# Performance work log

Measured on AMD Instinct MI355X. Metric: run time of the kernel, lower is better.

## Reference

```python
import jax, jax.numpy as jnp
import numpy as np
from math import sqrt

D_MODEL = 1024
N_HEADS = 16
FFN = 4096
B, N = 2, 2048
EPS = 1e-5


def _layernorm(x, g, b):
    mu = jnp.mean(x, -1, keepdims=True)
    var = jnp.mean((x - mu) ** 2, -1, keepdims=True)
    return (x - mu) * jax.lax.rsqrt(var + EPS) * g + b


def setup_inputs() -> dict:
    key = jax.random.key(0)
    ks = jax.random.split(key, 12)
    s = 1.0 / sqrt(D_MODEL)
    sf = 1.0 / sqrt(FFN)
    inp = {
        "tgt": jax.random.normal(ks[0], (B, N, D_MODEL), jnp.float32),
        # True = masked. Causal: query i may attend to keys j <= i.
        "tgt_mask": jnp.triu(jnp.ones((N, N), jnp.bool_), k=1),
        "tgt_key_pad_mask": jnp.zeros((B, N), jnp.bool_),
        "Wq": jax.random.uniform(ks[1], (D_MODEL, D_MODEL), jnp.float32, -s, s),
        "Wk": jax.random.uniform(ks[2], (D_MODEL, D_MODEL), jnp.float32, -s, s),
        "Wv": jax.random.uniform(ks[3], (D_MODEL, D_MODEL), jnp.float32, -s, s),
        "Wo": jax.random.uniform(ks[4], (D_MODEL, D_MODEL), jnp.float32, -s, s),
        "bo": jax.random.uniform(ks[5], (D_MODEL,), jnp.float32, -s, s),
        "W1": jax.random.uniform(ks[6], (FFN, D_MODEL), jnp.float32, -s, s),
        "b1": jax.random.uniform(ks[7], (FFN,), jnp.float32, -s, s),
        "W2": jax.random.uniform(ks[8], (D_MODEL, FFN), jnp.float32, -sf, sf),
        "b2": jax.random.uniform(ks[9], (D_MODEL,), jnp.float32, -sf, sf),
        "g1": jnp.ones((D_MODEL,), jnp.float32),
        "beta1": jnp.zeros((D_MODEL,), jnp.float32),
        "g2": jnp.ones((D_MODEL,), jnp.float32),
        "beta2": jnp.zeros((D_MODEL,), jnp.float32),
    }
    return inp


def _mha(x, tgt_mask, pad_mask, Wq, Wk, Wv, Wo, bo):
    b, n, d = x.shape
    dk = d // N_HEADS
    q = (x @ Wq.T).reshape(b, n, N_HEADS, dk).transpose(0, 2, 1, 3)  # bhnd
    k = (x @ Wk.T).reshape(b, n, N_HEADS, dk).transpose(0, 2, 1, 3)
    v = (x @ Wv.T).reshape(b, n, N_HEADS, dk).transpose(0, 2, 1, 3)
    scores = jnp.einsum("bhqd,bhkd->bhqk", q, k) / sqrt(dk)
    mask = tgt_mask[None, None, :, :] | pad_mask[:, None, None, :]
    scores = jnp.where(mask, -jnp.inf, scores)
    att = jax.nn.softmax(scores, axis=-1)
    out = jnp.einsum("bhqk,bhkd->bhqd", att, v).transpose(0, 2, 1, 3).reshape(b, n, d)
    return out @ Wo.T + bo


def reference(tgt, tgt_mask, tgt_key_pad_mask, Wq, Wk, Wv, Wo, bo,
              W1, b1, W2, b2, g1, beta1, g2, beta2):
    # PostNorm logic (pre_norm=False), dropout=0 (eval)
    h = _mha(tgt, tgt_mask, tgt_key_pad_mask, Wq, Wk, Wv, Wo, bo)
    x = _layernorm(tgt + h, g1, beta1)
    m = jax.nn.gelu(x @ W1.T + b1, approximate=True) @ W2.T + b2
    return _layernorm(x + m, g2, beta2)
```

## Files before the change

kernel.cpp:

```cpp
#include <hip/hip_runtime.h>


#define DEV __device__ __forceinline__

typedef __attribute__((ext_vector_type(4)))  float f32x4;
typedef __attribute__((ext_vector_type(16))) float f32x16;
typedef __attribute__((ext_vector_type(8)))  short s16x8;

static constexpr int Bb   = 2;
static constexpr int NN   = 2048;
static constexpr int DM   = 1024;
static constexpr int HH   = 16;
static constexpr int DK   = 64;
static constexpr int FF   = 4096;
static constexpr int ROWS = Bb * NN;

#define AS1(p) ((const __attribute__((address_space(1))) void*)(p))
#define AS3(p) ((__attribute__((address_space(3))) void*)(p))

DEV unsigned short f2bf(float f) {
  unsigned u = __float_as_uint(f);
  u += 0x7fff + ((u >> 16) & 1);
  return (unsigned short)(u >> 16);
}
DEV float fexp2(float x) {
  float r;
  asm("v_exp_f32 %0, %1" : "=v"(r) : "v"(x));
  return r;
}
DEV unsigned cvtpk(float lo, float hi) {
  unsigned r;
  asm("v_cvt_pk_bf16_f32 %0, %1, %2" : "=v"(r) : "v"(lo), "v"(hi));
  return r;
}

__global__ __launch_bounds__(256) void k_cast7(
    const float* __restrict__ tgt, const float* __restrict__ Wq,
    const float* __restrict__ Wk, const float* __restrict__ Wv,
    const float* __restrict__ Wo, const float* __restrict__ W1,
    const float* __restrict__ W2,
    ushort* __restrict__ xb, ushort* __restrict__ wqb,
    ushort* __restrict__ w1b, ushort* __restrict__ w2b) {
  const int i = blockIdx.x * 256 + threadIdx.x;
  constexpr int S0 = 1048576;
  constexpr int S1 = 262144;
  const float4* src;
  ushort* dstp;
  if (i < S0)               { src = (const float4*)tgt + i;            dstp = xb  + (size_t)i * 4; }
  else if (i < S0 + S1)     { src = (const float4*)Wq + (i - S0);      dstp = wqb + (size_t)(i - S0) * 4; }
  else if (i < S0 + 2 * S1) { src = (const float4*)Wk + (i - S0 - S1); dstp = wqb + (size_t)(i - S0) * 4; }
  else if (i < S0 + 3 * S1) { src = (const float4*)Wv + (i - S0 - 2 * S1); dstp = wqb + (size_t)(i - S0) * 4; }
  else if (i < S0 + 4 * S1) { src = (const float4*)Wo + (i - S0 - 3 * S1); dstp = wqb + (size_t)(i - S0) * 4; }
  else if (i < 3 * S0)      { src = (const float4*)W1 + (i - 2 * S0);  dstp = w1b + (size_t)(i - 2 * S0) * 4; }
  else                      { src = (const float4*)W2 + (i - 3 * S0);  dstp = w2b + (size_t)(i - 3 * S0) * 4; }
  float4 v = *src;
  ushort4 o;
  o.x = f2bf(v.x); o.y = f2bf(v.y); o.z = f2bf(v.z); o.w = f2bf(v.w);
  *reinterpret_cast<ushort4*>(dstp) = o;
}

template <int EPI, int BN, bool QKV, int SPLITK>
__global__ __launch_bounds__(256) void k_gemm(
    const ushort* __restrict__ A, const ushort* __restrict__ Bt,
    const float* __restrict__ bias, const float* __restrict__ resid,
    ushort* __restrict__ Cb, float* __restrict__ Cf,
    int K, int nbx) {
  __shared__ ushort As[2][128][32];
  __shared__ ushort Bs[2][BN][32];

  const int t = threadIdx.x;
  const int lane = t & 63, w = t >> 6;
  const int lr = lane & 15, lg = lane >> 4;
  const int lrow = lane >> 2, lc8 = (lane & 3) * 8;

  const int nwg = gridDim.x;
  const int bid = blockIdx.x;
  const int q8 = nwg >> 3, r8 = nwg & 7;
  const int xcd = bid & 7, lin = bid >> 3;
  int wg = (xcd < r8 ? xcd * (q8 + 1) : r8 * (q8 + 1) + (xcd - r8) * q8) + lin;
  int kc = 0;
  if constexpr (SPLITK == 2) { kc = wg & 1; wg >>= 1; }
  const int band = wg / (4 * nbx);
  const int inn  = wg % (4 * nbx);
  const int by = band * 4 + (inn & 3);
  const int bx = inn >> 2;

  const int bRow = by * 128;
  const int bCol = bx * BN;
  const int Kc = K / SPLITK;
  const int kofs = kc * Kc;
  const int nk = Kc / 32;

  constexpr int NW = BN / 32;
  const int wRow = (w >> 1) * 64, wCol = (w & 1) * (BN / 2);

  const f32x4 zero = {0.f, 0.f, 0.f, 0.f};
  f32x4 acc[4][NW];
#pragma unroll
  for (int m = 0; m < 4; ++m)
#pragma unroll
    for (int n = 0; n < NW; ++n) acc[m][n] = zero;

  auto stage = [&](int buf, int tile) {
    const int kb = kofs + tile * 32;
#pragma unroll
    for (int i = 0; i < 2; ++i) {
      int rr = w * 32 + i * 16;
      __builtin_amdgcn_global_load_lds(
          AS1(A + (size_t)(bRow + rr + lrow) * K + kb + lc8),
          AS3(&As[buf][rr][0]), 16, 0, 0);
    }
#pragma unroll
    for (int i = 0; i < BN / 64; ++i) {
      int rr = w * (BN / 4) + i * 16;
      __builtin_amdgcn_global_load_lds(
          AS1(Bt + (size_t)(bCol + rr + lrow) * K + kb + lc8),
          AS3(&Bs[buf][rr][0]), 16, 0, 0);
    }
  };

  stage(0, 0);
  for (int tt = 0; tt < nk; ++tt) {
    const int cur = tt & 1;
    if (tt + 1 < nk) {
      stage(cur ^ 1, tt + 1);
      if constexpr (BN == 128) asm volatile("s_waitcnt vmcnt(4)" ::: "memory");
      else                     asm volatile("s_waitcnt vmcnt(3)" ::: "memory");
    } else {
      asm volatile("s_waitcnt vmcnt(0)" ::: "memory");
    }
    __builtin_amdgcn_s_barrier();
    __builtin_amdgcn_sched_barrier(0);

    s16x8 af[4], bfr[NW];
#pragma unroll
    for (int m = 0; m < 4; ++m)
      af[m] = *reinterpret_cast<const s16x8*>(&As[cur][wRow + m * 16 + lr][lg * 8]);
#pragma unroll
    for (int n = 0; n < NW; ++n)
      bfr[n] = *reinterpret_cast<const s16x8*>(&Bs[cur][wCol + n * 16 + lr][lg * 8]);
#pragma unroll
    for (int m = 0; m < 4; ++m)
#pragma unroll
      for (int n = 0; n < NW; ++n)
        acc[m][n] = __builtin_amdgcn_mfma_f32_16x16x32_bf16(af[m], bfr[n], acc[m][n], 0, 0, 0);

    asm volatile("s_waitcnt lgkmcnt(0)" ::: "memory");
    __builtin_amdgcn_s_barrier();
    __builtin_amdgcn_sched_barrier(0);
  }

  ushort* CbOut = Cb;
  int colBase = bCol, Ncols = nbx * BN, third = 0;
  if (QKV) {
    third = bCol >> 10;
    CbOut = Cb + (size_t)third * ROWS * DM;
    colBase = bCol & 1023;
    Ncols = DM;
  }
#pragma unroll
  for (int m = 0; m < 4; ++m) {
    int gr = bRow + wRow + m * 16 + lg * 4;
#pragma unroll
    for (int n = 0; n < NW; ++n) {
      int gc = colBase + wCol + n * 16 + lr;
      if (QKV && third == 2) {
        int h = gc >> 6, d = gc & 63;
        int b = gr >> 11, ntok = gr & (NN - 1);
        size_t basev = ((size_t)(b * HH + h) * DK + d) * NN;
        int nb = ntok & ~63, c = (ntok >> 3) & 7, j0 = ntok & 7;
        ushort4 ov;
        ov.x = f2bf(acc[m][n][0]);
        ov.y = f2bf(acc[m][n][1]);
        ov.z = f2bf(acc[m][n][2]);
        ov.w = f2bf(acc[m][n][3]);
        ushort* VT = Cb + (size_t)3 * ROWS * DM;
        *reinterpret_cast<ushort4*>(VT + basev + nb + ((c ^ (d & 7)) << 3) + j0) = ov;
        continue;
      }
      float bv = (EPI == 1 || EPI == 2) ? bias[gc] : 0.0f;
#pragma unroll
      for (int r = 0; r < 4; ++r) {
        int nr = gr + r;
        float v = acc[m][n][r] + bv;
        if (EPI == 3) {
          Cf[((size_t)kc * ROWS + nr) * Ncols + gc] = v;
        } else if (EPI == 2) {
          size_t idx = (size_t)nr * Ncols + gc;
          Cf[idx] = v + resid[idx];
        } else if (EPI == 1) {
          size_t idx = (size_t)nr * Ncols + gc;
          float u = v + 0.044715f * v * v * v;
          float g = v / (1.0f + __expf(-1.5957691216057308f * u));
          CbOut[idx] = f2bf(g);
        } else {
          int gcs = gc;
          if (QKV && third == 1)
            gcs = (gc & ~63) | ((gc ^ ((nr & 7) << 3)) & 63);
          CbOut[(size_t)nr * Ncols + gcs] = f2bf(v);
        }
      }
    }
  }
}

template <int WB, int RED>
__global__ __launch_bounds__(256) void k_ln(const float* __restrict__ in,
                                            const float* __restrict__ p0,
                                            const float* __restrict__ p1,
                                            const float* __restrict__ pb,
                                            const float* __restrict__ g,
                                            const float* __restrict__ bta,
                                            float* __restrict__ outf,
                                            ushort* __restrict__ outb) {
  const int row = blockIdx.x;
  const int t = threadIdx.x;
  float4 v = reinterpret_cast<const float4*>(in + (size_t)row * DM)[t];
  if (RED) {
    float4 a = reinterpret_cast<const float4*>(p0 + (size_t)row * DM)[t];
    float4 b = reinterpret_cast<const float4*>(p1 + (size_t)row * DM)[t];
    float4 c = reinterpret_cast<const float4*>(pb)[t];
    v.x += a.x + b.x + c.x;
    v.y += a.y + b.y + c.y;
    v.z += a.z + b.z + c.z;
    v.w += a.w + b.w + c.w;
  }
  float s1 = v.x + v.y + v.z + v.w;
  float s2 = v.x * v.x + v.y * v.y + v.z * v.z + v.w * v.w;
#pragma unroll
  for (int m = 32; m; m >>= 1) {
    s1 += __shfl_xor(s1, m, 64);
    s2 += __shfl_xor(s2, m, 64);
  }
  __shared__ float red[2][4];
  if ((t & 63) == 0) { red[0][t >> 6] = s1; red[1][t >> 6] = s2; }
  __syncthreads();
  s1 = red[0][0] + red[0][1] + red[0][2] + red[0][3];
  s2 = red[1][0] + red[1][1] + red[1][2] + red[1][3];
  const float mu = s1 * (1.0f / DM);
  const float var = s2 * (1.0f / DM) - mu * mu;
  const float rstd = rsqrtf(var + 1e-5f);
  float4 gv = reinterpret_cast<const float4*>(g)[t];
  float4 bv = reinterpret_cast<const float4*>(bta)[t];
  float4 o;
  o.x = (v.x - mu) * rstd * gv.x + bv.x;
  o.y = (v.y - mu) * rstd * gv.y + bv.y;
  o.z = (v.z - mu) * rstd * gv.z + bv.z;
  o.w = (v.w - mu) * rstd * gv.w + bv.w;
  reinterpret_cast<float4*>(outf + (size_t)row * DM)[t] = o;
  if (WB) {
    ushort4 ob;
    ob.x = f2bf(o.x); ob.y = f2bf(o.y); ob.z = f2bf(o.z); ob.w = f2bf(o.w);
    reinterpret_cast<ushort4*>(outb + (size_t)row * DM)[t] = ob;
  }
}

static __device__ const unsigned char SCHED40[40][2] = {
  {15,0},{15,1},{15,2},{15,3}, {14,0},{14,1},{14,2},{14,3},
  {13,0},{13,1},{13,2},{13,3}, {12,0},{12,1},{12,2},{12,3},
  {11,0},{11,1},{11,2}, {10,0},{10,1},{10,2},
  {9,0},{9,1},{9,2}, {8,0},{8,1},{8,2},
  {7,0},{7,1}, {6,0},{6,1}, {5,0},{5,1}, {4,0},{4,1},
  {3,0},{2,0},{1,0},{0,0}};

__global__ __launch_bounds__(256) void k_attn(const ushort* __restrict__ Q,
                                              const ushort* __restrict__ Kb,
                                              const ushort* __restrict__ vT,
                                              ushort* __restrict__ O,
                                              float* __restrict__ Op,
                                              float* __restrict__ ml) {
  __shared__ ushort Ks[2][64 * 64];
  __shared__ ushort Vs[2][64 * 64];

  const int t = threadIdx.x;
  const int bid = blockIdx.x;
  const int xcd = bid & 7, j = bid >> 3;
  const int head = j & 3, e = j >> 2;
  const int qi = SCHED40[e][0], seg = SCHED40[e][1];
  const int bh = xcd * 4 + head;
  const int ntiles = 2 * qi + 2;
  const int nseg = (2 * qi + 9) >> 3;
  const int tb = ntiles / nseg, rem = ntiles % nseg;
  const int kt0 = seg * tb + (seg < rem ? seg : rem);
  const int kt1 = kt0 + tb + (seg < rem ? 1 : 0);

  const int lane = t & 63, wid = t >> 6;
  const int l31 = lane & 31, hi = lane >> 5;
  const int q0w = qi * 128 + wid * 32;
  const size_t qbase = ((size_t)(bh >> 4) * NN) * DM + (bh & 15) * DK;
  const size_t vbase = (size_t)bh * DK * NN;

  const float C = 0.18033688011112043f;

  s16x8 qf[4];
#pragma unroll
  for (int c = 0; c < 4; ++c)
    qf[c] = *reinterpret_cast<const s16x8*>(Q + qbase + (size_t)(q0w + l31) * DM + c * 16 + hi * 8);

  float mrun = -1e30f, lrun = 0.f, negcm = 1e30f;
  f32x16 accO[2];
#pragma unroll
  for (int dt = 0; dt < 2; ++dt)
#pragma unroll
    for (int r = 0; r < 16; ++r) accO[dt][r] = 0.f;

  auto stage = [&](int buf, int kt) {
    const int kk = kt * 64;
#pragma unroll
    for (int i = 0; i < 2; ++i) {
      int row0 = wid * 16 + i * 8;
      __builtin_amdgcn_global_load_lds(
          AS1(Kb + qbase + (size_t)(kk + row0 + (lane >> 3)) * DM + (lane & 7) * 8),
          AS3(&Ks[buf][row0 * 64]), 16, 0, 0);
      __builtin_amdgcn_global_load_lds(
          AS1(vT + vbase + (size_t)(row0 + (lane >> 3)) * NN + kk + (lane & 7) * 8),
          AS3(&Vs[buf][row0 * 64]), 16, 0, 0);
    }
  };

  stage(0, kt0);
  for (int kt = kt0, li = 0; kt < kt1; ++kt, ++li) {
    const int cur = li & 1;
    const int kk = kt * 64;
    __syncthreads();
    if (kt + 1 < kt1) stage(cur ^ 1, kt + 1);

    if (kk <= q0w + 31) {
      const char* KsB = (const char*)Ks[cur];
      const char* VsB = (const char*)Vs[cur];
      const bool diag = (kk + 64 > q0w);
      const int nsub = (kk + 32 <= q0w + 31) ? 2 : 1;

      f32x16 st[2];
      __builtin_amdgcn_s_setprio(1);
#pragma unroll
      for (int sub = 0; sub < 2; ++sub) {
        if (sub >= nsub) break;
#pragma unroll
        for (int r = 0; r < 16; ++r) st[sub][r] = 0.f;
        const int row = sub * 32 + l31;
        const int swz = (row & 7) << 4;
#pragma unroll
        for (int c = 0; c < 4; ++c) {
          s16x8 kf = *reinterpret_cast<const s16x8*>(KsB + row * 128 + ((c * 32 + hi * 16) ^ swz));
          st[sub] = __builtin_amdgcn_mfma_f32_32x32x16_bf16(kf, qf[c], st[sub], 0, 0, 0);
        }
      }
      __builtin_amdgcn_s_setprio(0);

      const int q = q0w + l31;
      float p[32];
#pragma unroll
      for (int sub = 0; sub < 2; ++sub) {
        if (sub >= nsub) break;
#pragma unroll
        for (int r = 0; r < 16; ++r) {
          float v = st[sub][r];
          if (diag) {
            int kl = sub * 32 + (r & 3) + 8 * (r >> 2) + 4 * hi;
            if (kk + kl > q) v = -1e30f;
          }
          p[sub * 16 + r] = v;
        }
      }
      float a[16];
#pragma unroll
      for (int i = 0; i < 16; ++i) a[i] = (nsub == 2) ? fmaxf(p[i], p[i + 16]) : p[i];
#pragma unroll
      for (int s = 8; s; s >>= 1)
#pragma unroll
        for (int i = 0; i < 8; ++i) if (i < s) a[i] = fmaxf(a[i], a[i + s]);
      float rm = fmaxf(a[0], __shfl_xor(a[0], 32, 64));

      if (__any(rm > mrun)) {
        const float mn = fmaxf(mrun, rm);
        const float alpha = fexp2(C * (mrun - mn));
        mrun = mn;
        negcm = -C * mn;
        lrun *= alpha;
#pragma unroll
        for (int dt = 0; dt < 2; ++dt) accO[dt] *= alpha;
      }

#pragma unroll
      for (int sub = 0; sub < 2; ++sub) {
        if (sub >= nsub) break;
#pragma unroll
        for (int i = 0; i < 16; ++i)
          p[sub * 16 + i] = fexp2(fmaf(p[sub * 16 + i], C, negcm));
      }
#pragma unroll
      for (int i = 0; i < 16; ++i) a[i] = (nsub == 2) ? (p[i] + p[i + 16]) : p[i];
#pragma unroll
      for (int s = 8; s; s >>= 1)
#pragma unroll
        for (int i = 0; i < 8; ++i) if (i < s) a[i] += a[i + s];
      lrun += a[0] + __shfl_xor(a[0], 32, 64);

      s16x8 pf[4];
#pragma unroll
      for (int sub = 0; sub < 2; ++sub) {
        if (sub >= nsub) break;
#pragma unroll
        for (int hf = 0; hf < 2; ++hf) {
          const float* pp = &p[sub * 16 + hf * 8];
          unsigned X0 = cvtpk(pp[0], pp[1]);
          unsigned X1 = cvtpk(pp[2], pp[3]);
          unsigned Y0 = cvtpk(pp[4], pp[5]);
          unsigned Y1 = cvtpk(pp[6], pp[7]);
          asm volatile("v_permlane32_swap_b32 %0, %1" : "+v"(X0), "+v"(Y0));
          asm volatile("v_permlane32_swap_b32 %0, %1" : "+v"(X1), "+v"(Y1));
          union { unsigned u[4]; s16x8 v; } uu;
          uu.u[0] = X0; uu.u[1] = X1; uu.u[2] = Y0; uu.u[3] = Y1;
          pf[sub * 2 + hf] = uu.v;
        }
      }

      __builtin_amdgcn_s_setprio(1);
#pragma unroll
      for (int dt = 0; dt < 2; ++dt) {
        const int d = dt * 32 + l31;
        const int vswz = (d & 7) << 4;
#pragma unroll
        for (int kc = 0; kc < 4; ++kc) {
          if (kc >= nsub * 2) break;
          s16x8 vf = *reinterpret_cast<const s16x8*>(VsB + d * 128 + ((kc * 32 + hi * 16) ^ vswz));
          accO[dt] = __builtin_amdgcn_mfma_f32_32x32x16_bf16(vf, pf[kc], accO[dt], 0, 0, 0);
        }
      }
      __builtin_amdgcn_s_setprio(0);
    }
  }

  if (nseg == 1) {
    const int q = q0w + l31;
    const float inv = 1.0f / lrun;
#pragma unroll
    for (int dt = 0; dt < 2; ++dt)
#pragma unroll
      for (int rg = 0; rg < 4; ++rg) {
        int d0 = 8 * rg + 4 * hi + 32 * dt;
        ushort4 ov;
        ov.x = f2bf(accO[dt][rg * 4 + 0] * inv);
        ov.y = f2bf(accO[dt][rg * 4 + 1] * inv);
        ov.z = f2bf(accO[dt][rg * 4 + 2] * inv);
        ov.w = f2bf(accO[dt][rg * 4 + 3] * inv);
        *reinterpret_cast<ushort4*>(O + qbase + (size_t)q * DM + d0) = ov;
      }
  } else {
    const int pidx = (bh * 12 + (qi - 4)) * 4 + seg;
    float* op = Op + (size_t)pidx * (128 * 64);
    const int row = wid * 32 + l31;
#pragma unroll
    for (int dt = 0; dt < 2; ++dt)
#pragma unroll
      for (int rg = 0; rg < 4; ++rg) {
        int d0 = 8 * rg + 4 * hi + 32 * dt;
        f32x4 v4 = { accO[dt][rg * 4 + 0], accO[dt][rg * 4 + 1],
                     accO[dt][rg * 4 + 2], accO[dt][rg * 4 + 3] };
        *reinterpret_cast<f32x4*>(op + (size_t)row * 64 + d0) = v4;
      }
    if (hi == 0) {
      ml[(size_t)pidx * 256 + row * 2 + 0] = mrun;
      ml[(size_t)pidx * 256 + row * 2 + 1] = lrun;
    }
  }
}

__global__ __launch_bounds__(256) void k_amerge(const float* __restrict__ Op,
                                                const float* __restrict__ ml,
                                                ushort* __restrict__ O) {
  const int bid = blockIdx.x;
  const int bh = bid / 12, qq = bid % 12;
  const int qi = qq + 4;
  const int nseg = (2 * qi + 9) >> 3;
  const int t = threadIdx.x;
  const int row = t >> 1, dh = (t & 1) * 32;
  const float C = 0.18033688011112043f;
  const int pbase = (bh * 12 + qq) * 4;

  float M = -1e30f;
  for (int s = 0; s < nseg; ++s)
    M = fmaxf(M, ml[(size_t)(pbase + s) * 256 + row * 2 + 0]);
  float wsum = 0.f;
  for (int s = 0; s < nseg; ++s) {
    float ms = ml[(size_t)(pbase + s) * 256 + row * 2 + 0];
    float ls = ml[(size_t)(pbase + s) * 256 + row * 2 + 1];
    wsum += ls * fexp2(C * (ms - M));
  }
  const float inv = 1.0f / wsum;

  f32x4 acc[8];
#pragma unroll
  for (int i = 0; i < 8; ++i) acc[i] = (f32x4){0.f, 0.f, 0.f, 0.f};
  for (int s = 0; s < nseg; ++s) {
    float wsc = fexp2(C * (ml[(size_t)(pbase + s) * 256 + row * 2 + 0] - M));
    const float* os = Op + (size_t)(pbase + s) * (128 * 64) + (size_t)row * 64 + dh;
#pragma unroll
    for (int i = 0; i < 8; ++i) {
      f32x4 v = reinterpret_cast<const f32x4*>(os)[i];
      acc[i] += v * wsc;
    }
  }

  const int b = bh >> 4, h = bh & 15;
  const int n = qi * 128 + row;
  ushort* dst = O + ((size_t)(b * NN + n)) * DM + h * DK + dh;
#pragma unroll
  for (int i = 0; i < 8; ++i) {
    ushort4 ov;
    ov.x = f2bf(acc[i][0] * inv);
    ov.y = f2bf(acc[i][1] * inv);
    ov.z = f2bf(acc[i][2] * inv);
    ov.w = f2bf(acc[i][3] * inv);
    reinterpret_cast<ushort4*>(dst)[i] = ov;
  }
}

extern "C" void kernel_launch(void* const* d_in, const int* in_sizes, int n_in,
                              void* d_out, int out_size, void* d_ws, size_t ws_size,
                              hipStream_t stream) {
  const float* tgt = (const float*)d_in[0];
  const float* Wq  = (const float*)d_in[3];
  const float* Wk  = (const float*)d_in[4];
  const float* Wv  = (const float*)d_in[5];
  const float* Wo  = (const float*)d_in[6];
  const float* bo  = (const float*)d_in[7];
  const float* W1  = (const float*)d_in[8];
  const float* b1  = (const float*)d_in[9];
  const float* W2  = (const float*)d_in[10];
  const float* b2  = (const float*)d_in[11];
  const float* g1  = (const float*)d_in[12];
  const float* be1 = (const float*)d_in[13];
  const float* g2  = (const float*)d_in[14];
  const float* be2 = (const float*)d_in[15];

  char* ws = (char*)d_ws;
  size_t off = 0;
  auto alloc = [&](size_t bytes) {
    void* p = ws + off;
    off += (bytes + 255) & ~(size_t)255;
    return p;
  };
  ushort* xb   = (ushort*)alloc((size_t)ROWS * DM * 2);
  ushort* wqb  = (ushort*)alloc((size_t)DM * DM * 2);
  ushort* wkb  = (ushort*)alloc((size_t)DM * DM * 2);
  ushort* wvb  = (ushort*)alloc((size_t)DM * DM * 2);
  ushort* wob  = (ushort*)alloc((size_t)DM * DM * 2);
  ushort* w1b  = (ushort*)alloc((size_t)FF * DM * 2);
  ushort* w2b  = (ushort*)alloc((size_t)DM * FF * 2);
  ushort* qbuf = (ushort*)alloc((size_t)ROWS * DM * 2);
  ushort* kbuf = (ushort*)alloc((size_t)ROWS * DM * 2);
  ushort* vbuf = (ushort*)alloc((size_t)ROWS * DM * 2);
  ushort* vtb  = (ushort*)alloc((size_t)ROWS * DM * 2);
  ushort* atnb = (ushort*)alloc((size_t)ROWS * DM * 2);
  float*  h1   = (float*)alloc((size_t)ROWS * DM * 4);
  float*  x1f  = (float*)alloc((size_t)ROWS * DM * 4);
  ushort* x1b  = (ushort*)alloc((size_t)ROWS * DM * 2);
  ushort* t1b  = (ushort*)alloc((size_t)ROWS * FF * 2);
  float*  mlb  = (float*)alloc((size_t)1536 * 256 * 4);
  float*  Opb  = h1;
  float*  pp   = (float*)qbuf;
  (void)ws_size; (void)in_sizes; (void)n_in; (void)out_size;
  (void)wkb; (void)wvb; (void)kbuf; (void)vbuf; (void)vtb;

  dim3 blk(256);
  k_cast7<<<dim3(16384), blk, 0, stream>>>(tgt, Wq, Wk, Wv, Wo, W1, W2,
                                           xb, wqb, w1b, w2b);

  k_gemm<0, 128, true, 1><<<dim3(24 * 32), blk, 0, stream>>>(
      xb, wqb, nullptr, nullptr, qbuf, nullptr, DM, 24);

  k_attn<<<dim3(1280), blk, 0, stream>>>(qbuf, kbuf, vtb, atnb, Opb, mlb);
  k_amerge<<<dim3(384), blk, 0, stream>>>(Opb, mlb, atnb);

  k_gemm<2, 64, false, 1><<<dim3(16 * 32), blk, 0, stream>>>(
      atnb, wob, bo, tgt, nullptr, h1, DM, 16);
  k_ln<1, 0><<<dim3(ROWS), blk, 0, stream>>>(h1, nullptr, nullptr, nullptr,
                                             g1, be1, x1f, x1b);

  k_gemm<1, 128, false, 1><<<dim3(32 * 32), blk, 0, stream>>>(
      x1b, w1b, b1, nullptr, t1b, nullptr, DM, 32);
  k_gemm<3, 64, false, 2><<<dim3(2 * 16 * 32), blk, 0, stream>>>(
      t1b, w2b, nullptr, nullptr, nullptr, pp, FF, 16);
  k_ln<0, 1><<<dim3(ROWS), blk, 0, stream>>>(x1f, pp, pp + (size_t)ROWS * DM, b2,
                                             g2, be2, (float*)d_out, nullptr);
}
```

Baseline: 263.3 us.

## Add 256x256-tile 8-wave GEMM kernel for QKV and FFN1 projections

Introduces a new GEMM kernel with 512 threads, 256x256 output tiles and BK=64. It uses a fragment-ordered LDS layout and interleaves the next-tile global-to-LDS loads across four compute phases, with s_setprio raised around the MFMA bursts. The QKV and FFN-up GEMMs now use this kernel to get more data reuse per tile, while the other GEMMs keep the old kernel with the now-unused epilogues removed. The trade-off is fewer workgroups (192 and 256 on a 256-CU part), which risks poor occupancy and tail imbalance, plus higher register pressure from the 8x4 accumulators.

```diff
diff --git a/kernel.cpp b/kernel.cpp
--- a/kernel.cpp
+++ b/kernel.cpp
@@ -59,99 +59,114 @@
   *reinterpret_cast<ushort4*>(dstp) = o;
 }
 
-template <int EPI, int BN, bool QKV, int SPLITK>
-__global__ __launch_bounds__(256) void k_gemm(
+template <int EPI, bool QKV>
+__global__ __launch_bounds__(512) void k_gemm8(
     const ushort* __restrict__ A, const ushort* __restrict__ Bt,
-    const float* __restrict__ bias, const float* __restrict__ resid,
-    ushort* __restrict__ Cb, float* __restrict__ Cf,
-    int K, int nbx) {
-  __shared__ ushort As[2][128][32];
-  __shared__ ushort Bs[2][BN][32];
+    const float* __restrict__ bias,
+    ushort* __restrict__ Cb, int K, int nbx) {
+  __shared__ ushort As[2][16384];
+  __shared__ ushort Bs[2][16384];
 
   const int t = threadIdx.x;
   const int lane = t & 63, w = t >> 6;
   const int lr = lane & 15, lg = lane >> 4;
-  const int lrow = lane >> 2, lc8 = (lane & 3) * 8;
+  const int wr = w >> 2, wc = w & 3;
 
   const int nwg = gridDim.x;
   const int bid = blockIdx.x;
   const int q8 = nwg >> 3, r8 = nwg & 7;
   const int xcd = bid & 7, lin = bid >> 3;
-  int wg = (xcd < r8 ? xcd * (q8 + 1) : r8 * (q8 + 1) + (xcd - r8) * q8) + lin;
-  int kc = 0;
-  if constexpr (SPLITK == 2) { kc = wg & 1; wg >>= 1; }
+  const int wg = (xcd < r8 ? xcd * (q8 + 1) : r8 * (q8 + 1) + (xcd - r8) * q8) + lin;
   const int band = wg / (4 * nbx);
   const int inn  = wg % (4 * nbx);
   const int by = band * 4 + (inn & 3);
   const int bx = inn >> 2;
 
-  const int bRow = by * 128;
-  const int bCol = bx * BN;
-  const int Kc = K / SPLITK;
-  const int kofs = kc * Kc;
-  const int nk = Kc / 32;
-
-  constexpr int NW = BN / 32;
-  const int wRow = (w >> 1) * 64, wCol = (w & 1) * (BN / 2);
-
-  const f32x4 zero = {0.f, 0.f, 0.f, 0.f};
-  f32x4 acc[4][NW];
-#pragma unroll
-  for (int m = 0; m < 4; ++m)
-#pragma unroll
-    for (int n = 0; n < NW; ++n) acc[m][n] = zero;
-
-  auto stage = [&](int buf, int tile) {
-    const int kb = kofs + tile * 32;
-#pragma unroll
-    for (int i = 0; i < 2; ++i) {
-      int rr = w * 32 + i * 16;
-      __builtin_amdgcn_global_load_lds(
-          AS1(A + (size_t)(bRow + rr + lrow) * K + kb + lc8),
-          AS3(&As[buf][rr][0]), 16, 0, 0);
-    }
-#pragma unroll
-    for (int i = 0; i < BN / 64; ++i) {
-      int rr = w * (BN / 4) + i * 16;
-      __builtin_amdgcn_global_load_lds(
-          AS1(Bt + (size_t)(bCol + rr + lrow) * K + kb + lc8),
-          AS3(&Bs[buf][rr][0]), 16, 0, 0);
-    }
+  const int bRow = by * 256;
+  const int bCol = bx * 256;
+  const int nk = K / 64;
+
+  f32x4 acc[8][4];
+#pragma unroll
+  for (int m = 0; m < 8; ++m)
+#pragma unroll
+    for (int n = 0; n < 4; ++n) acc[m][n] = (f32x4){0.f, 0.f, 0.f, 0.f};
+
+  char* AsB0 = (char*)As[0];
+  char* BsB0 = (char*)Bs[0];
+
+  auto stageAB = [&](int buf, int kb, int j) {
+    const int ca = w * 4 + j;
+    const int m16 = ca >> 1, ks = ca & 1;
+    __builtin_amdgcn_global_load_lds(
+        AS1(A + (size_t)(bRow + m16 * 16 + lr) * K + kb + ks * 32 + lg * 8),
+        AS3(AsB0 + buf * 32768 + ca * 1024), 16, 0, 0);
+    __builtin_amdgcn_global_load_lds(
+        AS1(Bt + (size_t)(bCol + m16 * 16 + lr) * K + kb + ks * 32 + lg * 8),
+        AS3(BsB0 + buf * 32768 + ca * 1024), 16, 0, 0);
   };
 
-  stage(0, 0);
+#pragma unroll
+  for (int j = 0; j < 4; ++j) stageAB(0, 0, j);
+  asm volatile("s_waitcnt vmcnt(0)" ::: "memory");
+  __builtin_amdgcn_s_barrier();
+  __builtin_amdgcn_sched_barrier(0);
+
+  s16x8 bfr[4][2];
+
   for (int tt = 0; tt < nk; ++tt) {
     const int cur = tt & 1;
-    if (tt + 1 < nk) {
-      stage(cur ^ 1, tt + 1);
-      if constexpr (BN == 128) asm volatile("s_waitcnt vmcnt(4)" ::: "memory");
-      else                     asm volatile("s_waitcnt vmcnt(3)" ::: "memory");
-    } else {
-      asm volatile("s_waitcnt vmcnt(0)" ::: "memory");
-    }
-    __builtin_amdgcn_s_barrier();
-    __builtin_amdgcn_sched_barrier(0);
-
-    s16x8 af[4], bfr[NW];
-#pragma unroll
-    for (int m = 0; m < 4; ++m)
-      af[m] = *reinterpret_cast<const s16x8*>(&As[cur][wRow + m * 16 + lr][lg * 8]);
-#pragma unroll
-    for (int n = 0; n < NW; ++n)
-      bfr[n] = *reinterpret_cast<const s16x8*>(&Bs[cur][wCol + n * 16 + lr][lg * 8]);
-#pragma unroll
-    for (int m = 0; m < 4; ++m)
-#pragma unroll
-      for (int n = 0; n < NW; ++n)
-        acc[m][n] = __builtin_amdgcn_mfma_f32_16x16x32_bf16(af[m], bfr[n], acc[m][n], 0, 0, 0);
-
-    asm volatile("s_waitcnt lgkmcnt(0)" ::: "memory");
-    __builtin_amdgcn_s_barrier();
-    __builtin_amdgcn_sched_barrier(0);
+    const bool last = (tt + 1 == nk);
+    const int kbn = (tt + 1) * 64;
+    const char* Ab = AsB0 + cur * 32768;
+    const char* Bb = BsB0 + cur * 32768;
+
+#pragma unroll
+    for (int p = 0; p < 4; ++p) {
+      if (p == 0) {
+#pragma unroll
+        for (int n = 0; n < 4; ++n)
+#pragma unroll
+          for (int ks = 0; ks < 2; ++ks)
+            bfr[n][ks] = *reinterpret_cast<const s16x8*>(
+                Bb + ((wc * 4 + n) * 2 + ks) * 1024 + lane * 16);
+      }
+      s16x8 af[2][2];
+#pragma unroll
+      for (int i = 0; i < 2; ++i)
+#pragma unroll
+        for (int ks = 0; ks < 2; ++ks)
+          af[i][ks] = *reinterpret_cast<const s16x8*>(
+              Ab + ((wr * 8 + 2 * p + i) * 2 + ks) * 1024 + lane * 16);
+
+      if (p < 2 && !last) {
+        stageAB(cur ^ 1, kbn, p * 2 + 0);
+        stageAB(cur ^ 1, kbn, p * 2 + 1);
+      }
+
+      __builtin_amdgcn_s_barrier();
+      asm volatile("s_waitcnt lgkmcnt(0)" ::: "memory");
+      __builtin_amdgcn_sched_barrier(0);
+
+      __builtin_amdgcn_s_setprio(1);
+#pragma unroll
+      for (int i = 0; i < 2; ++i)
+#pragma unroll
+        for (int n = 0; n < 4; ++n)
+#pragma unroll
+          for (int ks = 0; ks < 2; ++ks)
+            acc[2 * p + i][n] = __builtin_amdgcn_mfma_f32_16x16x32_bf16(
+                af[i][ks], bfr[n][ks], acc[2 * p + i][n], 0, 0, 0);
+      __builtin_amdgcn_s_setprio(0);
+
+      if (p == 3) asm volatile("s_waitcnt vmcnt(0)" ::: "memory");
+      __builtin_amdgcn_s_barrier();
+      __builtin_amdgcn_sched_barrier(0);
+    }
   }
 
   ushort* CbOut = Cb;
-  int colBase = bCol, Ncols = nbx * BN, third = 0;
+  int colBase = bCol, Ncols = nbx * 256, third = 0;
   if (QKV) {
     third = bCol >> 10;
     CbOut = Cb + (size_t)third * ROWS * DM;
@@ -159,11 +174,11 @@
     Ncols = DM;
   }
 #pragma unroll
-  for (int m = 0; m < 4; ++m) {
-    int gr = bRow + wRow + m * 16 + lg * 4;
-#pragma unroll
-    for (int n = 0; n < NW; ++n) {
-      int gc = colBase + wCol + n * 16 + lr;
+  for (int m = 0; m < 8; ++m) {
+    int gr = bRow + wr * 128 + m * 16 + lg * 4;
+#pragma unroll
+    for (int n = 0; n < 4; ++n) {
+      int gc = colBase + wc * 64 + n * 16 + lr;
       if (QKV && third == 2) {
         int h = gc >> 6, d = gc & 63;
         int b = gr >> 11, ntok = gr & (NN - 1);
@@ -178,26 +193,132 @@
         *reinterpret_cast<ushort4*>(VT + basev + nb + ((c ^ (d & 7)) << 3) + j0) = ov;
         continue;
       }
-      float bv = (EPI == 1 || EPI == 2) ? bias[gc] : 0.0f;
+      float bv = (EPI == 1) ? bias[gc] : 0.0f;
+#pragma unroll
+      for (int r = 0; r < 4; ++r) {
+        int nr = gr + r;
+        float v = acc[m][n][r] + bv;
+        if (EPI == 1) {
+          float u = v + 0.044715f * v * v * v;
+          float g = v / (1.0f + __expf(-1.5957691216057308f * u));
+          CbOut[(size_t)nr * Ncols + gc] = f2bf(g);
+        } else {
+          int gcs = gc;
+          if (QKV && third == 1)
+            gcs = (gc & ~63) | ((gc ^ ((nr & 7) << 3)) & 63);
+          CbOut[(size_t)nr * Ncols + gcs] = f2bf(v);
+        }
+      }
+    }
+  }
+}
+
+template <int EPI, int BN, int SPLITK>
+__global__ __launch_bounds__(256) void k_gemm(
+    const ushort* __restrict__ A, const ushort* __restrict__ Bt,
+    const float* __restrict__ bias, const float* __restrict__ resid,
+    float* __restrict__ Cf, int K, int nbx) {
+  __shared__ ushort As[2][128][32];
+  __shared__ ushort Bs[2][BN][32];
+
+  const int t = threadIdx.x;
+  const int lane = t & 63, w = t >> 6;
+  const int lr = lane & 15, lg = lane >> 4;
+  const int lrow = lane >> 2, lc8 = (lane & 3) * 8;
+
+  const int nwg = gridDim.x;
+  const int bid = blockIdx.x;
+  const int q8 = nwg >> 3, r8 = nwg & 7;
+  const int xcd = bid & 7, lin = bid >> 3;
+  int wg = (xcd < r8 ? xcd * (q8 + 1) : r8 * (q8 + 1) + (xcd - r8) * q8) + lin;
+  int kc = 0;
+  if constexpr (SPLITK == 2) { kc = wg & 1; wg >>= 1; }
+  const int band = wg / (4 * nbx);
+  const int inn  = wg % (4 * nbx);
+  const int by = band * 4 + (inn & 3);
+  const int bx = inn >> 2;
+
+  const int bRow = by * 128;
+  const int bCol = bx * BN;
+  const int Kc = K / SPLITK;
+  const int kofs = kc * Kc;
+  const int nk = Kc / 32;
+
+  constexpr int NW = BN / 32;
+  const int wRow = (w >> 1) * 64, wCol = (w & 1) * (BN / 2);
+
+  f32x4 acc[4][NW];
+#pragma unroll
+  for (int m = 0; m < 4; ++m)
+#pragma unroll
+    for (int n = 0; n < NW; ++n) acc[m][n] = (f32x4){0.f, 0.f, 0.f, 0.f};
+
+  auto stage = [&](int buf, int tile) {
+    const int kb = kofs + tile * 32;
+#pragma unroll
+    for (int i = 0; i < 2; ++i) {
+      int rr = w * 32 + i * 16;
+      __builtin_amdgcn_global_load_lds(
+          AS1(A + (size_t)(bRow + rr + lrow) * K + kb + lc8),
+          AS3(&As[buf][rr][0]), 16, 0, 0);
+    }
+#pragma unroll
+    for (int i = 0; i < BN / 64; ++i) {
+      int rr = w * (BN / 4) + i * 16;
+      __builtin_amdgcn_global_load_lds(
+          AS1(Bt + (size_t)(bCol + rr + lrow) * K + kb + lc8),
+          AS3(&Bs[buf][rr][0]), 16, 0, 0);
+    }
+  };
+
+  stage(0, 0);
+  for (int tt = 0; tt < nk; ++tt) {
+    const int cur = tt & 1;
+    if (tt + 1 < nk) {
+      stage(cur ^ 1, tt + 1);
+      if constexpr (BN == 128) asm volatile("s_waitcnt vmcnt(4)" ::: "memory");
+      else                     asm volatile("s_waitcnt vmcnt(3)" ::: "memory");
+    } else {
+      asm volatile("s_waitcnt vmcnt(0)" ::: "memory");
+    }
+    __builtin_amdgcn_s_barrier();
+    __builtin_amdgcn_sched_barrier(0);
+
+    s16x8 af[4], bfr[NW];
+#pragma unroll
+    for (int m = 0; m < 4; ++m)
+      af[m] = *reinterpret_cast<const s16x8*>(&As[cur][wRow + m * 16 + lr][lg * 8]);
+#pragma unroll
+    for (int n = 0; n < NW; ++n)
+      bfr[n] = *reinterpret_cast<const s16x8*>(&Bs[cur][wCol + n * 16 + lr][lg * 8]);
+#pragma unroll
+    for (int m = 0; m < 4; ++m)
+#pragma unroll
+      for (int n = 0; n < NW; ++n)
+        acc[m][n] = __builtin_amdgcn_mfma_f32_16x16x32_bf16(af[m], bfr[n], acc[m][n], 0, 0, 0);
+
+    asm volatile("s_waitcnt lgkmcnt(0)" ::: "memory");
+    __builtin_amdgcn_s_barrier();
+    __builtin_amdgcn_sched_barrier(0);
+  }
+
+  const int Ncols = nbx * BN;
+#pragma unroll
+  for (int m = 0; m < 4; ++m) {
+    int gr = bRow + wRow + m * 16 + lg * 4;
+#pragma unroll
+    for (int n = 0; n < NW; ++n) {
+      int gc = bCol + wCol + n * 16 + lr;
+      float bv = (EPI == 2) ? bias[gc] : 0.0f;
 #pragma unroll
       for (int r = 0; r < 4; ++r) {
         int nr = gr + r;
         float v = acc[m][n][r] + bv;
         if (EPI == 3) {
           Cf[((size_t)kc * ROWS + nr) * Ncols + gc] = v;
-        } else if (EPI == 2) {
+        } else {
           size_t idx = (size_t)nr * Ncols + gc;
           Cf[idx] = v + resid[idx];
-        } else if (EPI == 1) {
-          size_t idx = (size_t)nr * Ncols + gc;
-          float u = v + 0.044715f * v * v * v;
-          float g = v / (1.0f + __expf(-1.5957691216057308f * u));
-          CbOut[idx] = f2bf(g);
-        } else {
-          int gcs = gc;
-          if (QKV && third == 1)
-            gcs = (gc & ~63) | ((gc ^ ((nr & 7) << 3)) & 63);
-          CbOut[(size_t)nr * Ncols + gcs] = f2bf(v);
         }
       }
     }
@@ -568,21 +689,22 @@
   k_cast7<<<dim3(16384), blk, 0, stream>>>(tgt, Wq, Wk, Wv, Wo, W1, W2,
                                            xb, wqb, w1b, w2b);
 
-  k_gemm<0, 128, true, 1><<<dim3(24 * 32), blk, 0, stream>>>(
-      xb, wqb, nullptr, nullptr, qbuf, nullptr, DM, 24);
+  k_gemm8<0, true><<<dim3(192), dim3(512), 0, stream>>>(
+      xb, wqb, nullptr, qbuf, DM, 12);
 
   k_attn<<<dim3(1280), blk, 0, stream>>>(qbuf, kbuf, vtb, atnb, Opb, mlb);
   k_amerge<<<dim3(384), blk, 0, stream>>>(Opb, mlb, atnb);
 
-  k_gemm<2, 64, false, 1><<<dim3(16 * 32), blk, 0, stream>>>(
-      atnb, wob, bo, tgt, nullptr, h1, DM, 16);
+  k_gemm<2, 64, 1><<<dim3(16 * 32), blk, 0, stream>>>(
+      atnb, wob, bo, tgt, h1, DM, 16);
   k_ln<1, 0><<<dim3(ROWS), blk, 0, stream>>>(h1, nullptr, nullptr, nullptr,
                                              g1, be1, x1f, x1b);
 
-  k_gemm<1, 128, false, 1><<<dim3(32 * 32), blk, 0, stream>>>(
-      x1b, w1b, b1, nullptr, t1b, nullptr, DM, 32);
-  k_gemm<3, 64, false, 2><<<dim3(2 * 16 * 32), blk, 0, stream>>>(
-      t1b, w2b, nullptr, nullptr, nullptr, pp, FF, 16);
+  k_gemm8<1, false><<<dim3(256), dim3(512), 0, stream>>>(
+      x1b, w1b, b1, t1b, DM, 16);
+
+  k_gemm<3, 64, 2><<<dim3(2 * 16 * 32), blk, 0, stream>>>(
+      t1b, w2b, nullptr, nullptr, pp, FF, 16);
   k_ln<0, 1><<<dim3(ROWS), blk, 0, stream>>>(x1f, pp, pp + (size_t)ROWS * DM, b2,
                                              g2, be2, (float*)d_out, nullptr);
 }
```

After: 289.3 us. 1.1x slower.
